# Performance work log

Hardware: AMD Instinct MI355X
Metric: run time of the kernel (lower is better)

Reference implementation:

```python
import jax, jax.numpy as jnp
import numpy as np

N_NODES = 50000
N_EDGES = 600000
D_IN = 256    # hidden_lstm
D_GNN = 128   # hidden_gnn
D_OUT = 1     # out_channels


def setup_inputs() -> dict:
    key = jax.random.key(0)
    ks = jax.random.split(key, 8)
    x = jax.random.normal(ks[0], (N_NODES, D_IN), dtype=jnp.float32)
    edge_index = jax.random.randint(ks[1], (2, N_EDGES), 0, N_NODES, dtype=jnp.int32)
    # SAGEConv params: lin_l applied to aggregated neighbors (with bias), lin_r to root
    s_in = 1.0 / np.sqrt(D_IN)
    W_l = jax.random.uniform(ks[2], (D_IN, D_GNN), jnp.float32, -s_in, s_in)
    b_l = jax.random.uniform(ks[3], (D_GNN,), jnp.float32, -s_in, s_in)
    W_r = jax.random.uniform(ks[4], (D_IN, D_GNN), jnp.float32, -s_in, s_in)
    # fc head
    s_g = 1.0 / np.sqrt(D_GNN)
    W_fc = jax.random.uniform(ks[5], (D_GNN, D_OUT), jnp.float32, -s_g, s_g)
    b_fc = jax.random.uniform(ks[6], (D_OUT,), jnp.float32, -s_g, s_g)
    return {"x": x, "edge_index": edge_index, "W_l": W_l, "b_l": b_l,
            "W_r": W_r, "W_fc": W_fc, "b_fc": b_fc}


def reference(x, edge_index, W_l, b_l, W_r, W_fc, b_fc):
    # SAGEConv, aggr='mean': out = lin_l(mean_{j in N(i)} x_j) + lin_r(x_i)
    src = edge_index[0]  # message source
    dst = edge_index[1]  # message target
    n = x.shape[0]
    agg = jax.ops.segment_sum(x[src], dst, num_segments=n)            # [N, D_IN]
    cnt = jax.ops.segment_sum(jnp.ones((src.shape[0], 1), x.dtype), dst,
                              num_segments=n)                         # [N, 1]
    mean = agg / jnp.maximum(cnt, 1.0)
    h = mean @ W_l + b_l + x @ W_r                                    # [N, D_GNN]
    pred = jax.nn.sigmoid(h @ W_fc + b_fc).squeeze()                  # [N]
    return h, pred
```

## Files before the change

kernel.cpp:

```cpp
#include <hip/hip_runtime.h>
#include <hip/hip_bf16.h>
#include <math.h>

#define N_NODES 50000
#define N_EDGES 600000
#define D_IN 256
#define D_GNN 128
#define CAP 32
#define MAX_OVER 8192
#define EB_STRIDE 264

typedef short s16x8 __attribute__((ext_vector_type(8)));
typedef float f32x4 __attribute__((ext_vector_type(4)));

__device__ __forceinline__ unsigned short f2bf(float f) {
  unsigned int u = __float_as_uint(f);
  u += 0x7FFFu + ((u >> 16) & 1u);
  return (unsigned short)(u >> 16);
}

__global__ __launch_bounds__(256) void pack0(
    const float* __restrict__ Wl, const float* __restrict__ Wr,
    ushort* __restrict__ Wcp, int* __restrict__ cursor,
    int* __restrict__ ovcnt) {
  int i = blockIdx.x * 256 + threadIdx.x;
  if (i < N_NODES) cursor[i] = 0;
  if (i == 0) ovcnt[0] = 0;
  if (i < 8192) {
    int q = i & 3, col = (i >> 2) & 255, ks = i >> 10;
    const float* W = (col < 128) ? Wl : Wr;
    int c = col & 127;
    int k0 = ks * 32 + q * 8;
    s16x8 v;
#pragma unroll
    for (int j = 0; j < 8; j++) v[j] = (short)f2bf(W[(k0 + j) * D_GNN + c]);
    *((s16x8*)(Wcp + (size_t)i * 8)) = v;
  }
}

__global__ __launch_bounds__(512, 4) void fused_gemm_fill(
    const float* __restrict__ x, const ushort* __restrict__ Wcp,
    const float* __restrict__ b_l, const int* __restrict__ ei,
    int* __restrict__ cursor, int* __restrict__ colp,
    int* __restrict__ ovcnt, int2* __restrict__ over,
    ushort* __restrict__ yb, ushort* __restrict__ yrb) {
  __shared__ float xs[64 * 256];
  const int t = threadIdx.x;
  const int n0 = blockIdx.x * 64;
  const int l = t & 63;
  const int w = t >> 6;

#pragma unroll
  for (int j = 0; j < 8; j++) {
    const int row = j * 8 + w;
    int gn = n0 + row;
    if (gn >= N_NODES) gn = N_NODES - 1;
    const int sc = (l & ~7) | ((l & 7) ^ (row & 7));
    __builtin_amdgcn_global_load_lds(
        (const __attribute__((address_space(1))) unsigned int*)(
            x + (size_t)gn * 256 + sc * 4),
        (__attribute__((address_space(3))) unsigned int*)(xs + row * 256),
        16, 0, 0);
  }

  {
    const int stride = gridDim.x * 512;
    for (int e = blockIdx.x * 512 + t; e < N_EDGES; e += stride) {
      int src = ei[e];
      int dst = ei[N_EDGES + e];
      int pos = atomicAdd(&cursor[dst], 1);
      if (pos < CAP) {
        colp[dst * CAP + pos] = src;
      } else {
        int o = atomicAdd(ovcnt, 1);
        if (o < MAX_OVER) over[o] = make_int2(dst, src);
      }
    }
  }

  const int wrow = w & 1;
  const int wcol = w >> 1;
  const int lq = l >> 4, l16 = l & 15;

  f32x4 acc[2][4];
#pragma unroll
  for (int a = 0; a < 2; a++)
#pragma unroll
    for (int b = 0; b < 4; b++) acc[a][b] = (f32x4){0.f, 0.f, 0.f, 0.f};

  const float* ap0[2];
  const float* ap1[2];
#pragma unroll
  for (int nt = 0; nt < 2; nt++) {
    int rl = wrow * 32 + nt * 16 + l16;
    int o0 = (lq * 2) ^ (rl & 7);
    ap0[nt] = xs + rl * 256 + o0 * 4;
    ap1[nt] = xs + rl * 256 + (o0 ^ 1) * 4;
  }
  const ushort* bptr[4];
#pragma unroll
  for (int ct = 0; ct < 4; ct++) {
    int col = wcol * 64 + ct * 16 + l16;
    bptr[ct] = Wcp + ((size_t)col * 4 + lq) * 8;
  }

  s16x8 B[4], Bn[4];
#pragma unroll
  for (int ct = 0; ct < 4; ct++) B[ct] = *((const s16x8*)(bptr[ct]));

  __syncthreads();

  union { s16x8 v; ushort4 u[2]; } ua;
#pragma unroll
  for (int ks = 0; ks < 8; ks++) {
    s16x8 A[2];
#pragma unroll
    for (int nt = 0; nt < 2; nt++) {
      float4 a0 = *((const float4*)(ap0[nt] + ks * 32));
      float4 a1 = *((const float4*)(ap1[nt] + ks * 32));
      __hip_bfloat162 h0 = __float22bfloat162_rn(make_float2(a0.x, a0.y));
      __hip_bfloat162 h1 = __float22bfloat162_rn(make_float2(a0.z, a0.w));
      __hip_bfloat162 h2 = __float22bfloat162_rn(make_float2(a1.x, a1.y));
      __hip_bfloat162 h3 = __float22bfloat162_rn(make_float2(a1.z, a1.w));
      ua.u[0] = *(ushort4*)&h0;
      ua.u[0].z = ((ushort2*)&h1)->x; ua.u[0].w = ((ushort2*)&h1)->y;
      ua.u[1].x = ((ushort2*)&h2)->x; ua.u[1].y = ((ushort2*)&h2)->y;
      ua.u[1].z = ((ushort2*)&h3)->x; ua.u[1].w = ((ushort2*)&h3)->y;
      A[nt] = ua.v;
    }
    if (ks < 7) {
#pragma unroll
      for (int ct = 0; ct < 4; ct++)
        Bn[ct] = *((const s16x8*)(bptr[ct] + (size_t)(ks + 1) * 256 * 32));
    }
#pragma unroll
    for (int nt = 0; nt < 2; nt++)
#pragma unroll
      for (int ct = 0; ct < 4; ct++)
        acc[nt][ct] = __builtin_amdgcn_mfma_f32_16x16x32_bf16(
            A[nt], B[ct], acc[nt][ct], 0, 0, 0);
#pragma unroll
    for (int ct = 0; ct < 4; ct++) B[ct] = Bn[ct];
  }

  __syncthreads();
  ushort* eb = (ushort*)xs;
#pragma unroll
  for (int nt = 0; nt < 2; nt++) {
#pragma unroll
    for (int ct = 0; ct < 4; ct++) {
      int col = wcol * 64 + ct * 16 + l16;
      float bias = (col >= 128) ? b_l[col - 128] : 0.f;
#pragma unroll
      for (int r = 0; r < 4; r++) {
        int rl = wrow * 32 + nt * 16 + lq * 4 + r;
        eb[rl * EB_STRIDE + col] = f2bf(acc[nt][ct][r] + bias);
      }
    }
  }
  __syncthreads();
#pragma unroll
  for (int p = 0; p < 4; p++) {
    int id2 = p * 512 + t;
    int rl = id2 >> 5;
    int c8 = (id2 & 31) * 8;
    int gn = n0 + rl;
    if (gn < N_NODES) {
      s16x8 v = *((const s16x8*)(eb + rl * EB_STRIDE + c8));
      if (c8 < 128)
        *((s16x8*)(yb + (size_t)gn * D_GNN + c8)) = v;
      else
        *((s16x8*)(yrb + (size_t)gn * D_GNN + (c8 - 128))) = v;
    }
  }
}

__global__ __launch_bounds__(256) void gather_pred(
    const int* __restrict__ cursor, const int* __restrict__ colp,
    const int* __restrict__ ovcnt, const int2* __restrict__ over,
    const ushort* __restrict__ yb, const ushort* __restrict__ yrb,
    const float* __restrict__ Wfc, const float* __restrict__ bfc,
    float* __restrict__ h, float* __restrict__ pred) {
  const int node = (blockIdx.x * 256 + threadIdx.x) >> 6;
  const int lane = threadIdx.x & 63;
  if (node >= N_NODES) return;
  const int degt = cursor[node];
  const int m = min(degt, CAP);
  float ax = 0.f, ay = 0.f;
  const unsigned int* y32 = (const unsigned int*)yb;

  int c = (lane < m) ? colp[node * CAP + lane] : 0;
  int j = 0;
  for (; j + 4 <= m; j += 4) {
    int s0 = __shfl(c, j), s1 = __shfl(c, j + 1);
    int s2 = __shfl(c, j + 2), s3 = __shfl(c, j + 3);
    unsigned int v0 = y32[(size_t)s0 * 64 + lane];
    unsigned int v1 = y32[(size_t)s1 * 64 + lane];
    unsigned int v2 = y32[(size_t)s2 * 64 + lane];
    unsigned int v3 = y32[(size_t)s3 * 64 + lane];
    ax += __uint_as_float(v0 << 16) + __uint_as_float(v1 << 16) +
          __uint_as_float(v2 << 16) + __uint_as_float(v3 << 16);
    ay += __uint_as_float(v0 & 0xFFFF0000u) + __uint_as_float(v1 & 0xFFFF0000u) +
          __uint_as_float(v2 & 0xFFFF0000u) + __uint_as_float(v3 & 0xFFFF0000u);
  }
  for (; j < m; j++) {
    int s0 = __shfl(c, j);
    unsigned int v0 = y32[(size_t)s0 * 64 + lane];
    ax += __uint_as_float(v0 << 16);
    ay += __uint_as_float(v0 & 0xFFFF0000u);
  }
  if (degt > CAP) {
    int nov = min(ovcnt[0], MAX_OVER);
    for (int k = 0; k < nov; k++) {
      int2 ov = over[k];
      if (ov.x == node) {
        unsigned int v0 = y32[(size_t)ov.y * 64 + lane];
        ax += __uint_as_float(v0 << 16);
        ay += __uint_as_float(v0 & 0xFFFF0000u);
      }
    }
  }

  const float ic = degt > 0 ? 1.f / (float)degt : 0.f;
  unsigned int yrv = ((const unsigned int*)yrb)[(size_t)node * 64 + lane];
  float h0 = ax * ic + __uint_as_float(yrv << 16);
  float h1 = ay * ic + __uint_as_float(yrv & 0xFFFF0000u);
  float2 hv; hv.x = h0; hv.y = h1;
  ((float2*)h)[(size_t)node * 64 + lane] = hv;
  float s = h0 * Wfc[2 * lane] + h1 * Wfc[2 * lane + 1];
#pragma unroll
  for (int off = 32; off > 0; off >>= 1) s += __shfl_down(s, off);
  if (lane == 0) pred[node] = 1.f / (1.f + expf(-(s + bfc[0])));
}

extern "C" void kernel_launch(void* const* d_in, const int* in_sizes, int n_in,
                              void* d_out, int out_size, void* d_ws,
                              size_t ws_size, hipStream_t stream) {
  const float* x   = (const float*)d_in[0];
  const int*   ei  = (const int*)d_in[1];
  const float* Wl  = (const float*)d_in[2];
  const float* bl  = (const float*)d_in[3];
  const float* Wr  = (const float*)d_in[4];
  const float* Wfc = (const float*)d_in[5];
  const float* bfc = (const float*)d_in[6];

  float* out  = (float*)d_out;
  float* h    = out;
  float* pred = out + (size_t)N_NODES * D_GNN;

  ushort* Wcp   = (ushort*)d_ws;
  ushort* yb    = Wcp + 8192 * 8;
  ushort* yrb   = yb + (size_t)N_NODES * D_GNN;
  int*   cursor = (int*)(yrb + (size_t)N_NODES * D_GNN);
  int*   ovcnt  = cursor + N_NODES;
  int2*  over   = (int2*)(ovcnt + 1);
  int*   colp   = (int*)(over + MAX_OVER);

  pack0<<<(N_NODES + 255) / 256, 256, 0, stream>>>(Wl, Wr, Wcp, cursor, ovcnt);

  fused_gemm_fill<<<(N_NODES + 63) / 64, 512, 0, stream>>>(
      x, Wcp, bl, ei, cursor, colp, ovcnt, over, yb, yrb);

  gather_pred<<<(N_NODES * 64 + 255) / 256, 256, 0, stream>>>(
      cursor, colp, ovcnt, over, yb, yrb, Wfc, bfc, h, pred);
}
```

Baseline: 174.7 us.

## Shrink GEMM tile to 16 rows, drop LDS staging, assign one edge per thread

The fused GEMM and CSR-fill kernel now runs with 16-row tiles and 256 threads per block. Each wave reads its A fragments straight from global memory instead of staging the tile through LDS, and each thread handles exactly one edge. The edge atomic is issued after the MFMA loop and the colp store after the epilogue write, so the atomic latency can overlap other work. Neighbor indices are stored as 16-bit values to halve colp traffic. In exchange, every block reloads the full packed weight matrix from cache, four times as many blocks as before.

```diff
diff --git a/kernel.cpp b/kernel.cpp
--- a/kernel.cpp
+++ b/kernel.cpp
@@ -38,132 +38,92 @@
   }
 }
 
-__global__ __launch_bounds__(512, 4) void fused_gemm_fill(
+__global__ __launch_bounds__(256, 6) void fused_gemm_fill(
     const float* __restrict__ x, const ushort* __restrict__ Wcp,
     const float* __restrict__ b_l, const int* __restrict__ ei,
-    int* __restrict__ cursor, int* __restrict__ colp,
+    int* __restrict__ cursor, ushort* __restrict__ colp,
     int* __restrict__ ovcnt, int2* __restrict__ over,
     ushort* __restrict__ yb, ushort* __restrict__ yrb) {
-  __shared__ float xs[64 * 256];
+  __shared__ ushort eb[16 * EB_STRIDE];
   const int t = threadIdx.x;
-  const int n0 = blockIdx.x * 64;
+  const int n0 = blockIdx.x * 16;
   const int l = t & 63;
   const int w = t >> 6;
-
-#pragma unroll
-  for (int j = 0; j < 8; j++) {
-    const int row = j * 8 + w;
-    int gn = n0 + row;
-    if (gn >= N_NODES) gn = N_NODES - 1;
-    const int sc = (l & ~7) | ((l & 7) ^ (row & 7));
-    __builtin_amdgcn_global_load_lds(
-        (const __attribute__((address_space(1))) unsigned int*)(
-            x + (size_t)gn * 256 + sc * 4),
-        (__attribute__((address_space(3))) unsigned int*)(xs + row * 256),
-        16, 0, 0);
-  }
-
-  {
-    const int stride = gridDim.x * 512;
-    for (int e = blockIdx.x * 512 + t; e < N_EDGES; e += stride) {
-      int src = ei[e];
-      int dst = ei[N_EDGES + e];
-      int pos = atomicAdd(&cursor[dst], 1);
-      if (pos < CAP) {
-        colp[dst * CAP + pos] = src;
-      } else {
-        int o = atomicAdd(ovcnt, 1);
-        if (o < MAX_OVER) over[o] = make_int2(dst, src);
-      }
-    }
-  }
-
-  const int wrow = w & 1;
-  const int wcol = w >> 1;
   const int lq = l >> 4, l16 = l & 15;
 
-  f32x4 acc[2][4];
-#pragma unroll
-  for (int a = 0; a < 2; a++)
-#pragma unroll
-    for (int b = 0; b < 4; b++) acc[a][b] = (f32x4){0.f, 0.f, 0.f, 0.f};
-
-  const float* ap0[2];
-  const float* ap1[2];
-#pragma unroll
-  for (int nt = 0; nt < 2; nt++) {
-    int rl = wrow * 32 + nt * 16 + l16;
-    int o0 = (lq * 2) ^ (rl & 7);
-    ap0[nt] = xs + rl * 256 + o0 * 4;
-    ap1[nt] = xs + rl * 256 + (o0 ^ 1) * 4;
-  }
+  const int e = blockIdx.x * 256 + t;
+  int esrc = 0, edst = 0;
+  const bool has_e = (e < N_EDGES);
+  if (has_e) {
+    esrc = ei[e];
+    edst = ei[N_EDGES + e];
+  }
+
+  int row = n0 + l16;
+  if (row >= N_NODES) row = N_NODES - 1;
+  const float* arow = x + (size_t)row * D_IN + lq * 8;
+
   const ushort* bptr[4];
 #pragma unroll
   for (int ct = 0; ct < 4; ct++) {
-    int col = wcol * 64 + ct * 16 + l16;
+    int col = w * 64 + ct * 16 + l16;
     bptr[ct] = Wcp + ((size_t)col * 4 + lq) * 8;
   }
 
-  s16x8 B[4], Bn[4];
-#pragma unroll
-  for (int ct = 0; ct < 4; ct++) B[ct] = *((const s16x8*)(bptr[ct]));
+  f32x4 acc[4];
+#pragma unroll
+  for (int ct = 0; ct < 4; ct++) acc[ct] = (f32x4){0.f, 0.f, 0.f, 0.f};
+
+#pragma unroll
+  for (int ks = 0; ks < 8; ks++) {
+    float4 a0 = *((const float4*)(arow + ks * 32));
+    float4 a1 = *((const float4*)(arow + ks * 32 + 4));
+    union { s16x8 v; ushort4 u[2]; } ua;
+    __hip_bfloat162 h0 = __float22bfloat162_rn(make_float2(a0.x, a0.y));
+    __hip_bfloat162 h1 = __float22bfloat162_rn(make_float2(a0.z, a0.w));
+    __hip_bfloat162 h2 = __float22bfloat162_rn(make_float2(a1.x, a1.y));
+    __hip_bfloat162 h3 = __float22bfloat162_rn(make_float2(a1.z, a1.w));
+    ua.u[0].x = ((ushort2*)&h0)->x; ua.u[0].y = ((ushort2*)&h0)->y;
+    ua.u[0].z = ((ushort2*)&h1)->x; ua.u[0].w = ((ushort2*)&h1)->y;
+    ua.u[1].x = ((ushort2*)&h2)->x; ua.u[1].y = ((ushort2*)&h2)->y;
+    ua.u[1].z = ((ushort2*)&h3)->x; ua.u[1].w = ((ushort2*)&h3)->y;
+    s16x8 A = ua.v;
+#pragma unroll
+    for (int ct = 0; ct < 4; ct++) {
+      s16x8 B = *((const s16x8*)(bptr[ct] + (size_t)ks * 8192));
+      acc[ct] = __builtin_amdgcn_mfma_f32_16x16x32_bf16(A, B, acc[ct], 0, 0, 0);
+    }
+  }
+
+  int pos = -1;
+  if (has_e) pos = atomicAdd(&cursor[edst], 1);
+
+#pragma unroll
+  for (int ct = 0; ct < 4; ct++) {
+    int col = w * 64 + ct * 16 + l16;
+    float bias = (col >= 128) ? b_l[col - 128] : 0.f;
+#pragma unroll
+    for (int r = 0; r < 4; r++) {
+      eb[(lq * 4 + r) * EB_STRIDE + col] = f2bf(acc[ct][r] + bias);
+    }
+  }
+
+  if (pos >= 0) {
+    if (pos < CAP) {
+      colp[edst * CAP + pos] = (ushort)esrc;
+    } else {
+      int o = atomicAdd(ovcnt, 1);
+      if (o < MAX_OVER) over[o] = make_int2(edst, esrc);
+    }
+  }
 
   __syncthreads();
 
-  union { s16x8 v; ushort4 u[2]; } ua;
-#pragma unroll
-  for (int ks = 0; ks < 8; ks++) {
-    s16x8 A[2];
-#pragma unroll
-    for (int nt = 0; nt < 2; nt++) {
-      float4 a0 = *((const float4*)(ap0[nt] + ks * 32));
-      float4 a1 = *((const float4*)(ap1[nt] + ks * 32));
-      __hip_bfloat162 h0 = __float22bfloat162_rn(make_float2(a0.x, a0.y));
-      __hip_bfloat162 h1 = __float22bfloat162_rn(make_float2(a0.z, a0.w));
-      __hip_bfloat162 h2 = __float22bfloat162_rn(make_float2(a1.x, a1.y));
-      __hip_bfloat162 h3 = __float22bfloat162_rn(make_float2(a1.z, a1.w));
-      ua.u[0] = *(ushort4*)&h0;
-      ua.u[0].z = ((ushort2*)&h1)->x; ua.u[0].w = ((ushort2*)&h1)->y;
-      ua.u[1].x = ((ushort2*)&h2)->x; ua.u[1].y = ((ushort2*)&h2)->y;
-      ua.u[1].z = ((ushort2*)&h3)->x; ua.u[1].w = ((ushort2*)&h3)->y;
-      A[nt] = ua.v;
-    }
-    if (ks < 7) {
-#pragma unroll
-      for (int ct = 0; ct < 4; ct++)
-        Bn[ct] = *((const s16x8*)(bptr[ct] + (size_t)(ks + 1) * 256 * 32));
-    }
-#pragma unroll
-    for (int nt = 0; nt < 2; nt++)
-#pragma unroll
-      for (int ct = 0; ct < 4; ct++)
-        acc[nt][ct] = __builtin_amdgcn_mfma_f32_16x16x32_bf16(
-            A[nt], B[ct], acc[nt][ct], 0, 0, 0);
-#pragma unroll
-    for (int ct = 0; ct < 4; ct++) B[ct] = Bn[ct];
-  }
-
-  __syncthreads();
-  ushort* eb = (ushort*)xs;
-#pragma unroll
-  for (int nt = 0; nt < 2; nt++) {
-#pragma unroll
-    for (int ct = 0; ct < 4; ct++) {
-      int col = wcol * 64 + ct * 16 + l16;
-      float bias = (col >= 128) ? b_l[col - 128] : 0.f;
-#pragma unroll
-      for (int r = 0; r < 4; r++) {
-        int rl = wrow * 32 + nt * 16 + lq * 4 + r;
-        eb[rl * EB_STRIDE + col] = f2bf(acc[nt][ct][r] + bias);
-      }
-    }
-  }
-  __syncthreads();
-#pragma unroll
-  for (int p = 0; p < 4; p++) {
-    int id2 = p * 512 + t;
-    int rl = id2 >> 5;
-    int c8 = (id2 & 31) * 8;
+#pragma unroll
+  for (int p = 0; p < 2; p++) {
+    int id = p * 256 + t;
+    int rl = id >> 5;
+    int c8 = (id & 31) * 8;
     int gn = n0 + rl;
     if (gn < N_NODES) {
       s16x8 v = *((const s16x8*)(eb + rl * EB_STRIDE + c8));
@@ -176,7 +136,7 @@
 }
 
 __global__ __launch_bounds__(256) void gather_pred(
-    const int* __restrict__ cursor, const int* __restrict__ colp,
+    const int* __restrict__ cursor, const ushort* __restrict__ colp,
     const int* __restrict__ ovcnt, const int2* __restrict__ over,
     const ushort* __restrict__ yb, const ushort* __restrict__ yrb,
     const float* __restrict__ Wfc, const float* __restrict__ bfc,
@@ -189,7 +149,7 @@
   float ax = 0.f, ay = 0.f;
   const unsigned int* y32 = (const unsigned int*)yb;
 
-  int c = (lane < m) ? colp[node * CAP + lane] : 0;
+  int c = (lane < m) ? (int)colp[node * CAP + lane] : 0;
   int j = 0;
   for (; j + 4 <= m; j += 4) {
     int s0 = __shfl(c, j), s1 = __shfl(c, j + 1);
@@ -254,11 +214,11 @@
   int*   cursor = (int*)(yrb + (size_t)N_NODES * D_GNN);
   int*   ovcnt  = cursor + N_NODES;
   int2*  over   = (int2*)(ovcnt + 1);
-  int*   colp   = (int*)(over + MAX_OVER);
+  ushort* colp  = (ushort*)(over + MAX_OVER);
 
   pack0<<<(N_NODES + 255) / 256, 256, 0, stream>>>(Wl, Wr, Wcp, cursor, ovcnt);
 
-  fused_gemm_fill<<<(N_NODES + 63) / 64, 512, 0, stream>>>(
+  fused_gemm_fill<<<(N_NODES + 15) / 16, 256, 0, stream>>>(
       x, Wcp, bl, ei, cursor, colp, ovcnt, over, yb, yrb);
 
   gather_pred<<<(N_NODES * 64 + 255) / 256, 256, 0, stream>>>(
```

Result: slower. 192.9 us (+10.5%).
